# Kernel optimization log

Measured on AMD Instinct MI355X. Metric: run time of the kernel, lower is better.

The kernel has to match this reference:

```python
import jax, jax.numpy as jnp
import numpy as np

ROUTING_ITERS = 3
OUT_CAPS = 64
BETA_V = 1.0
BETA_A = 1.0
EPS = 1e-09


def l2_normalize(x, axis=-1, eps=1e-12):
    # matches tf.nn.l2_normalize: x / sqrt(max(sum(x^2), eps))
    sq = jnp.sum(jnp.square(x), axis=axis, keepdims=True)
    return x * jax.lax.rsqrt(jnp.maximum(sq, eps))


def setup_inputs() -> dict:
    key = jax.random.key(0)
    k1, k2 = jax.random.split(key)
    B, I, O, P = 32, 2048, OUT_CAPS, 16
    votes = jax.random.normal(k1, (B, I, O, P), dtype=jnp.float32)
    activations_in = jax.random.uniform(k2, (B, I), dtype=jnp.float32)
    return {"votes": votes, "activations_in": activations_in}


def reference(votes, activations_in):
    # votes: [B, I, O, P]; activations_in: [B, I]
    B, I, O, P = votes.shape
    A_h = jnp.full((B, O), 1.0 / O, dtype=votes.dtype)          # [B, O]
    Mu_h = l2_normalize(jnp.mean(votes, axis=1), axis=-1)        # [B, O, P]

    votes_norm = l2_normalize(votes, axis=-1)                    # [B, I, O, P]
    a_in = activations_in[:, :, None]                            # [B, I, 1]

    for _ in range(ROUTING_ITERS):
        # agreement cost
        dot = jnp.einsum('biop,bop->bio', votes_norm, Mu_h)      # [B, I, O]
        cost_v = (1.0 - jnp.square(dot)) * BETA_V
        cost_a = jnp.abs(a_in - A_h[:, None, :]) * BETA_A        # [B, I, O]
        log_posterior = -(cost_v + cost_a) + jnp.log(A_h + EPS)[:, None, :]
        R = jax.nn.softmax(log_posterior, axis=2)                # [B, I, O]

        # activation update
        R_sum = jnp.sum(R * a_in, axis=1)                        # [B, O]
        A_h = R_sum / (jnp.sum(R_sum, axis=1, keepdims=True) + EPS)
        A_h = jnp.clip(A_h, EPS, 1.0 - EPS)

        # pose update (weighted mean of votes)
        num = jnp.einsum('bio,biop->bop', R, votes)              # [B, O, P]
        den = jnp.sum(R, axis=1)[:, :, None] + EPS               # [B, O, 1]
        Mu_h = l2_normalize(num / den, axis=-1)

    return Mu_h, A_h
```

## Files before the change

kernel.cpp:

```cpp
#include <hip/hip_runtime.h>
#include <math.h>

#define NB 32
#define NI 2048
#define NO 64
#define NP 16
#define NBLK 32
#define EPSF 1e-9f

__device__ __forceinline__ float wave_sum64_shfl(float v) {
#pragma unroll
    for (int off = 32; off > 0; off >>= 1) v += __shfl_xor(v, off);
    return v;
}

__device__ __forceinline__ float wave_sum64_dpp(float v) {
    v += __int_as_float(__builtin_amdgcn_update_dpp(
        0, __float_as_int(v), 0x111, 0xf, 0xf, false));
    v += __int_as_float(__builtin_amdgcn_update_dpp(
        0, __float_as_int(v), 0x112, 0xf, 0xf, false));
    v += __int_as_float(__builtin_amdgcn_update_dpp(
        0, __float_as_int(v), 0x114, 0xf, 0xf, false));
    v += __int_as_float(__builtin_amdgcn_update_dpp(
        0, __float_as_int(v), 0x118, 0xf, 0xf, false));
    v += __int_as_float(__builtin_amdgcn_update_dpp(
        0, __float_as_int(v), 0x142, 0xa, 0xf, false));
    v += __int_as_float(__builtin_amdgcn_update_dpp(
        0, __float_as_int(v), 0x143, 0xc, 0xf, false));
    return __int_as_float(__builtin_amdgcn_readlane(__float_as_int(v), 63));
}

__global__ __launch_bounds__(256) void mean_accum_kernel(
        const float* __restrict__ votes, float* __restrict__ pm) {
    const int b    = blockIdx.y;
    const int bx   = blockIdx.x;
    const int wave = threadIdx.x >> 6;
    const int lane = threadIdx.x & 63;

    float s[NP];
#pragma unroll
    for (int p = 0; p < NP; ++p) s[p] = 0.f;

    const float* vbase =
        votes + (((size_t)b * NI + bx * 64 + wave) * NO + lane) * NP;
#pragma unroll 2
    for (int k = 0; k < 16; ++k) {
        const float4* vp =
            reinterpret_cast<const float4*>(vbase + (size_t)k * 4 * NO * NP);
        float4 v0 = vp[0], v1 = vp[1], v2 = vp[2], v3 = vp[3];
        s[0] += v0.x;  s[1] += v0.y;  s[2] += v0.z;  s[3] += v0.w;
        s[4] += v1.x;  s[5] += v1.y;  s[6] += v1.z;  s[7] += v1.w;
        s[8] += v2.x;  s[9] += v2.y;  s[10] += v2.z; s[11] += v2.w;
        s[12] += v3.x; s[13] += v3.y; s[14] += v3.z; s[15] += v3.w;
    }

    __shared__ float red[4][NO * NP];
#pragma unroll
    for (int p = 0; p < NP; ++p) red[wave][lane * NP + p] = s[p];
    __syncthreads();
    float* dst = pm + (size_t)(b * NBLK + bx) * (NO * NP);
    for (int e = threadIdx.x; e < NO * NP; e += 256)
        dst[e] = red[0][e] + red[1][e] + red[2][e] + red[3][e];
}

__global__ void mean_final_kernel(const float* __restrict__ pm,
                                  float* __restrict__ Mu, float* __restrict__ A) {
    const int b = blockIdx.x;
    const int o = threadIdx.x;
    float m[NP];
#pragma unroll
    for (int p = 0; p < NP; ++p) m[p] = 0.f;
    for (int bx = 0; bx < NBLK; ++bx) {
        const float4* q = reinterpret_cast<const float4*>(
            pm + (size_t)(b * NBLK + bx) * (NO * NP) + o * NP);
        float4 q0 = q[0], q1 = q[1], q2 = q[2], q3 = q[3];
        m[0] += q0.x;  m[1] += q0.y;  m[2] += q0.z;  m[3] += q0.w;
        m[4] += q1.x;  m[5] += q1.y;  m[6] += q1.z;  m[7] += q1.w;
        m[8] += q2.x;  m[9] += q2.y;  m[10] += q2.z; m[11] += q2.w;
        m[12] += q3.x; m[13] += q3.y; m[14] += q3.z; m[15] += q3.w;
    }
    float ssq = 0.f;
#pragma unroll
    for (int p = 0; p < NP; ++p) { m[p] *= (1.0f / NI); ssq += m[p] * m[p]; }
    float inv = rsqrtf(fmaxf(ssq, 1e-12f));
#pragma unroll
    for (int p = 0; p < NP; ++p)
        Mu[((size_t)b * NO + o) * NP + p] = m[p] * inv;
    A[b * NO + o] = 1.0f / (float)NO;
}

__global__ __launch_bounds__(256) void iter_accum_kernel(
        const float* __restrict__ votes, const float* __restrict__ act,
        const float* __restrict__ Mu, const float* __restrict__ A,
        float* __restrict__ ppn, float* __restrict__ ppd) {
    const int b    = blockIdx.y;
    const int bx   = blockIdx.x;
    const int wave = threadIdx.x >> 6;
    const int lane = threadIdx.x & 63;

    float mu[NP];
    {
        const float4* mp = reinterpret_cast<const float4*>(
            Mu + ((size_t)b * NO + lane) * NP);
        float4 m0 = mp[0], m1 = mp[1], m2 = mp[2], m3 = mp[3];
        mu[0] = m0.x;  mu[1] = m0.y;  mu[2] = m0.z;  mu[3] = m0.w;
        mu[4] = m1.x;  mu[5] = m1.y;  mu[6] = m1.z;  mu[7] = m1.w;
        mu[8] = m2.x;  mu[9] = m2.y;  mu[10] = m2.z; mu[11] = m2.w;
        mu[12] = m3.x; mu[13] = m3.y; mu[14] = m3.z; mu[15] = m3.w;
    }
    const float Ao   = A[b * NO + lane];
    const float logA = __logf(Ao + EPSF);

    float num[NP];
#pragma unroll
    for (int p = 0; p < NP; ++p) num[p] = 0.f;
    float den = 0.f, rs = 0.f;

    const float* vbase =
        votes + (((size_t)b * NI + bx * 64 + wave) * NO + lane) * NP;
    const float* abase = act + b * NI + bx * 64 + wave;

#pragma unroll 2
    for (int k = 0; k < 16; ++k) {
        const float4* vp =
            reinterpret_cast<const float4*>(vbase + (size_t)k * 4 * NO * NP);
        float4 v0 = vp[0], v1 = vp[1], v2 = vp[2], v3 = vp[3];

        float ssq = v0.x * v0.x + v0.y * v0.y + v0.z * v0.z + v0.w * v0.w
                  + v1.x * v1.x + v1.y * v1.y + v1.z * v1.z + v1.w * v1.w
                  + v2.x * v2.x + v2.y * v2.y + v2.z * v2.z + v2.w * v2.w
                  + v3.x * v3.x + v3.y * v3.y + v3.z * v3.z + v3.w * v3.w;
        float dt  = v0.x * mu[0]  + v0.y * mu[1]  + v0.z * mu[2]  + v0.w * mu[3]
                  + v1.x * mu[4]  + v1.y * mu[5]  + v1.z * mu[6]  + v1.w * mu[7]
                  + v2.x * mu[8]  + v2.y * mu[9]  + v2.z * mu[10] + v2.w * mu[11]
                  + v3.x * mu[12] + v3.y * mu[13] + v3.z * mu[14] + v3.w * mu[15];

        float dn = dt * __builtin_amdgcn_rsqf(fmaxf(ssq, 1e-12f));
        float a  = abase[4 * k];
        float lp = logA - (1.0f - dn * dn) - fabsf(a - Ao);
        float e  = __expf(lp);
        float R  = e * __builtin_amdgcn_rcpf(wave_sum64_dpp(e));

        rs  += R * a;
        den += R;
        num[0]  += R * v0.x; num[1]  += R * v0.y; num[2]  += R * v0.z; num[3]  += R * v0.w;
        num[4]  += R * v1.x; num[5]  += R * v1.y; num[6]  += R * v1.z; num[7]  += R * v1.w;
        num[8]  += R * v2.x; num[9]  += R * v2.y; num[10] += R * v2.z; num[11] += R * v2.w;
        num[12] += R * v3.x; num[13] += R * v3.y; num[14] += R * v3.z; num[15] += R * v3.w;
    }

    __shared__ float red[4][NO * 18];
    float* myred = &red[wave][lane * 18];
#pragma unroll
    for (int p = 0; p < NP; ++p) myred[p] = num[p];
    myred[16] = den;
    myred[17] = rs;
    __syncthreads();
    {
        float* dn_ = ppn + (size_t)(b * NBLK + bx) * (NO * NP);
        for (int e = threadIdx.x; e < NO * NP; e += 256) {
            int o = e >> 4, p = e & 15;
            dn_[e] = red[0][o * 18 + p] + red[1][o * 18 + p]
                   + red[2][o * 18 + p] + red[3][o * 18 + p];
        }
        float* dd_ = ppd + (size_t)(b * NBLK + bx) * (NO * 2);
        for (int e = threadIdx.x; e < NO * 2; e += 256) {
            int o = e >> 1, k = 16 + (e & 1);
            dd_[e] = red[0][o * 18 + k] + red[1][o * 18 + k]
                   + red[2][o * 18 + k] + red[3][o * 18 + k];
        }
    }
}

__global__ void finalize_kernel(const float* __restrict__ ppn,
                                const float* __restrict__ ppd,
                                float* __restrict__ Mu_out,
                                float* __restrict__ A_out) {
    const int b = blockIdx.x;
    const int o = threadIdx.x;
    float num[NP];
#pragma unroll
    for (int p = 0; p < NP; ++p) num[p] = 0.f;
    float den = 0.f, rs = 0.f;
    for (int bx = 0; bx < NBLK; ++bx) {
        const float4* q = reinterpret_cast<const float4*>(
            ppn + (size_t)(b * NBLK + bx) * (NO * NP) + o * NP);
        float4 q0 = q[0], q1 = q[1], q2 = q[2], q3 = q[3];
        num[0] += q0.x;  num[1] += q0.y;  num[2] += q0.z;  num[3] += q0.w;
        num[4] += q1.x;  num[5] += q1.y;  num[6] += q1.z;  num[7] += q1.w;
        num[8] += q2.x;  num[9] += q2.y;  num[10] += q2.z; num[11] += q2.w;
        num[12] += q3.x; num[13] += q3.y; num[14] += q3.z; num[15] += q3.w;
        const float2* d = reinterpret_cast<const float2*>(
            ppd + (size_t)(b * NBLK + bx) * (NO * 2) + o * 2);
        float2 dv = d[0];
        den += dv.x;
        rs  += dv.y;
    }
    float tot = wave_sum64_shfl(rs);
    float Anew = rs / (tot + EPSF);
    Anew = fminf(fmaxf(Anew, EPSF), 1.0f - EPSF);
    A_out[b * NO + o] = Anew;

    float inv_dn = 1.0f / (den + EPSF);
    float ssq = 0.f;
#pragma unroll
    for (int p = 0; p < NP; ++p) { num[p] *= inv_dn; ssq += num[p] * num[p]; }
    float inv = rsqrtf(fmaxf(ssq, 1e-12f));
#pragma unroll
    for (int p = 0; p < NP; ++p)
        Mu_out[((size_t)b * NO + o) * NP + p] = num[p] * inv;
}

extern "C" void kernel_launch(void* const* d_in, const int* in_sizes, int n_in,
                              void* d_out, int out_size, void* d_ws, size_t ws_size,
                              hipStream_t stream) {
    const float* votes = (const float*)d_in[0];
    const float* act   = (const float*)d_in[1];

    float* Mu_out = (float*)d_out;
    float* A_out  = (float*)d_out + NB * NO * NP;

    float* ws  = (float*)d_ws;
    float* ppn = ws;
    float* ppd = ws + NB * NBLK * 1024;
    float* Mu  = ppd + NB * NBLK * 128;
    float* A   = Mu + NB * NO * NP;

    dim3 grid(NBLK, NB);
    dim3 blk(256);

    mean_accum_kernel<<<grid, blk, 0, stream>>>(votes, ppn);
    mean_final_kernel<<<NB, NO, 0, stream>>>(ppn, Mu, A);

    for (int it = 0; it < 3; ++it) {
        iter_accum_kernel<<<grid, blk, 0, stream>>>(votes, act, Mu, A, ppn, ppd);
        float* mo = (it == 2) ? Mu_out : Mu;
        float* ao = (it == 2) ? A_out  : A;
        finalize_kernel<<<NB, NO, 0, stream>>>(ppn, ppd, mo, ao);
    }
}
```

Measured before the change: 512.8 us.

## Coalesce vote loads with quad-per-capsule mapping and finer I-blocking

Each lane now loads one float4 of a contiguous 1KB capsule row, so a wave's load is fully coalesced instead of each lane reading 64 strided bytes. Four lanes share one output capsule, and the dot products and squared norms are combined with DPP quad reductions. The I-block shrinks from 64 to 32, doubling the grid to 2048 blocks for more parallelism, and the finalize and mean kernels use 256 threads to reduce the partial sums. The trade-off is more partial-sum traffic and extra reduction instructions per vote.

```diff
diff --git a/kernel.cpp b/kernel.cpp
--- a/kernel.cpp
+++ b/kernel.cpp
@@ -5,7 +5,8 @@
 #define NI 2048
 #define NO 64
 #define NP 16
-#define NBLK 32
+#define IBLK 32
+#define NXB (NI / IBLK)
 #define EPSF 1e-9f
 
 __device__ __forceinline__ float wave_sum64_shfl(float v) {
@@ -14,201 +15,252 @@
     return v;
 }
 
+template <int CTRL, int RM, int BM>
+__device__ __forceinline__ float dppadd(float v) {
+    return v + __int_as_float(__builtin_amdgcn_update_dpp(
+        0, __float_as_int(v), CTRL, RM, BM, false));
+}
+
 __device__ __forceinline__ float wave_sum64_dpp(float v) {
-    v += __int_as_float(__builtin_amdgcn_update_dpp(
-        0, __float_as_int(v), 0x111, 0xf, 0xf, false));
-    v += __int_as_float(__builtin_amdgcn_update_dpp(
-        0, __float_as_int(v), 0x112, 0xf, 0xf, false));
-    v += __int_as_float(__builtin_amdgcn_update_dpp(
-        0, __float_as_int(v), 0x114, 0xf, 0xf, false));
-    v += __int_as_float(__builtin_amdgcn_update_dpp(
-        0, __float_as_int(v), 0x118, 0xf, 0xf, false));
-    v += __int_as_float(__builtin_amdgcn_update_dpp(
-        0, __float_as_int(v), 0x142, 0xa, 0xf, false));
-    v += __int_as_float(__builtin_amdgcn_update_dpp(
-        0, __float_as_int(v), 0x143, 0xc, 0xf, false));
+    v = dppadd<0x111, 0xf, 0xf>(v);
+    v = dppadd<0x112, 0xf, 0xf>(v);
+    v = dppadd<0x114, 0xf, 0xf>(v);
+    v = dppadd<0x118, 0xf, 0xf>(v);
+    v = dppadd<0x142, 0xa, 0xf>(v);
+    v = dppadd<0x143, 0xc, 0xf>(v);
     return __int_as_float(__builtin_amdgcn_readlane(__float_as_int(v), 63));
 }
 
+__device__ __forceinline__ float quad_sum4(float v) {
+    v = dppadd<0xB1, 0xf, 0xf>(v);
+    v = dppadd<0x4E, 0xf, 0xf>(v);
+    return v;
+}
+
 __global__ __launch_bounds__(256) void mean_accum_kernel(
-        const float* __restrict__ votes, float* __restrict__ pm) {
-    const int b    = blockIdx.y;
-    const int bx   = blockIdx.x;
-    const int wave = threadIdx.x >> 6;
-    const int lane = threadIdx.x & 63;
-
-    float s[NP];
-#pragma unroll
-    for (int p = 0; p < NP; ++p) s[p] = 0.f;
-
-    const float* vbase =
-        votes + (((size_t)b * NI + bx * 64 + wave) * NO + lane) * NP;
+        const float* __restrict__ votes, float* __restrict__ ppn) {
+    const int b  = blockIdx.y;
+    const int bx = blockIdx.x;
+    const int w  = threadIdx.x >> 6;
+    const int l  = threadIdx.x & 63;
+
+    const float4* vb = reinterpret_cast<const float4*>(votes)
+                     + (((size_t)b * NI + bx * IBLK + w * (IBLK / 4)) << 8) + l;
+
+    float s[16];
+#pragma unroll
+    for (int p = 0; p < 16; ++p) s[p] = 0.f;
+
 #pragma unroll 2
-    for (int k = 0; k < 16; ++k) {
-        const float4* vp =
-            reinterpret_cast<const float4*>(vbase + (size_t)k * 4 * NO * NP);
-        float4 v0 = vp[0], v1 = vp[1], v2 = vp[2], v3 = vp[3];
-        s[0] += v0.x;  s[1] += v0.y;  s[2] += v0.z;  s[3] += v0.w;
-        s[4] += v1.x;  s[5] += v1.y;  s[6] += v1.z;  s[7] += v1.w;
-        s[8] += v2.x;  s[9] += v2.y;  s[10] += v2.z; s[11] += v2.w;
+    for (int k = 0; k < IBLK / 4; ++k) {
+        const float4* pk = vb + ((size_t)k << 8);
+        float4 v0 = pk[0], v1 = pk[64], v2 = pk[128], v3 = pk[192];
+        s[0]  += v0.x; s[1]  += v0.y; s[2]  += v0.z; s[3]  += v0.w;
+        s[4]  += v1.x; s[5]  += v1.y; s[6]  += v1.z; s[7]  += v1.w;
+        s[8]  += v2.x; s[9]  += v2.y; s[10] += v2.z; s[11] += v2.w;
         s[12] += v3.x; s[13] += v3.y; s[14] += v3.z; s[15] += v3.w;
     }
 
     __shared__ float red[4][NO * NP];
-#pragma unroll
-    for (int p = 0; p < NP; ++p) red[wave][lane * NP + p] = s[p];
-    __syncthreads();
-    float* dst = pm + (size_t)(b * NBLK + bx) * (NO * NP);
+    float4* r4 = reinterpret_cast<float4*>(red[w]);
+    r4[0 * 64 + l] = make_float4(s[0], s[1], s[2], s[3]);
+    r4[1 * 64 + l] = make_float4(s[4], s[5], s[6], s[7]);
+    r4[2 * 64 + l] = make_float4(s[8], s[9], s[10], s[11]);
+    r4[3 * 64 + l] = make_float4(s[12], s[13], s[14], s[15]);
+    __syncthreads();
+    float* dst = ppn + (size_t)(b * NXB + bx) * (NO * NP);
     for (int e = threadIdx.x; e < NO * NP; e += 256)
         dst[e] = red[0][e] + red[1][e] + red[2][e] + red[3][e];
 }
 
-__global__ void mean_final_kernel(const float* __restrict__ pm,
-                                  float* __restrict__ Mu, float* __restrict__ A) {
+__global__ __launch_bounds__(256) void mean_final_kernel(
+        const float* __restrict__ ppn, float* __restrict__ Mu,
+        float* __restrict__ A) {
     const int b = blockIdx.x;
-    const int o = threadIdx.x;
-    float m[NP];
-#pragma unroll
-    for (int p = 0; p < NP; ++p) m[p] = 0.f;
-    for (int bx = 0; bx < NBLK; ++bx) {
+    const int w = threadIdx.x >> 6;
+    const int l = threadIdx.x & 63;
+
+    float m[16];
+#pragma unroll
+    for (int p = 0; p < 16; ++p) m[p] = 0.f;
+    for (int bx = w; bx < NXB; bx += 4) {
         const float4* q = reinterpret_cast<const float4*>(
-            pm + (size_t)(b * NBLK + bx) * (NO * NP) + o * NP);
+            ppn + (size_t)(b * NXB + bx) * (NO * NP) + l * NP);
         float4 q0 = q[0], q1 = q[1], q2 = q[2], q3 = q[3];
-        m[0] += q0.x;  m[1] += q0.y;  m[2] += q0.z;  m[3] += q0.w;
-        m[4] += q1.x;  m[5] += q1.y;  m[6] += q1.z;  m[7] += q1.w;
-        m[8] += q2.x;  m[9] += q2.y;  m[10] += q2.z; m[11] += q2.w;
+        m[0]  += q0.x; m[1]  += q0.y; m[2]  += q0.z; m[3]  += q0.w;
+        m[4]  += q1.x; m[5]  += q1.y; m[6]  += q1.z; m[7]  += q1.w;
+        m[8]  += q2.x; m[9]  += q2.y; m[10] += q2.z; m[11] += q2.w;
         m[12] += q3.x; m[13] += q3.y; m[14] += q3.z; m[15] += q3.w;
     }
-    float ssq = 0.f;
-#pragma unroll
-    for (int p = 0; p < NP; ++p) { m[p] *= (1.0f / NI); ssq += m[p] * m[p]; }
-    float inv = rsqrtf(fmaxf(ssq, 1e-12f));
-#pragma unroll
-    for (int p = 0; p < NP; ++p)
-        Mu[((size_t)b * NO + o) * NP + p] = m[p] * inv;
-    A[b * NO + o] = 1.0f / (float)NO;
+    __shared__ float red[4][NO * 17];
+#pragma unroll
+    for (int p = 0; p < 16; ++p) red[w][l * 17 + p] = m[p];
+    __syncthreads();
+    if (w == 0) {
+        float mm[16], ssq = 0.f;
+#pragma unroll
+        for (int p = 0; p < 16; ++p) {
+            mm[p] = (red[0][l * 17 + p] + red[1][l * 17 + p]
+                   + red[2][l * 17 + p] + red[3][l * 17 + p]) * (1.0f / NI);
+            ssq += mm[p] * mm[p];
+        }
+        float inv = rsqrtf(fmaxf(ssq, 1e-12f));
+        float4* mo = reinterpret_cast<float4*>(Mu + ((size_t)b * NO + l) * NP);
+        mo[0] = make_float4(mm[0] * inv, mm[1] * inv, mm[2] * inv, mm[3] * inv);
+        mo[1] = make_float4(mm[4] * inv, mm[5] * inv, mm[6] * inv, mm[7] * inv);
+        mo[2] = make_float4(mm[8] * inv, mm[9] * inv, mm[10] * inv, mm[11] * inv);
+        mo[3] = make_float4(mm[12] * inv, mm[13] * inv, mm[14] * inv, mm[15] * inv);
+        A[b * NO + l] = 1.0f / (float)NO;
+    }
 }
 
 __global__ __launch_bounds__(256) void iter_accum_kernel(
         const float* __restrict__ votes, const float* __restrict__ act,
         const float* __restrict__ Mu, const float* __restrict__ A,
         float* __restrict__ ppn, float* __restrict__ ppd) {
-    const int b    = blockIdx.y;
-    const int bx   = blockIdx.x;
-    const int wave = threadIdx.x >> 6;
-    const int lane = threadIdx.x & 63;
-
-    float mu[NP];
-    {
-        const float4* mp = reinterpret_cast<const float4*>(
-            Mu + ((size_t)b * NO + lane) * NP);
-        float4 m0 = mp[0], m1 = mp[1], m2 = mp[2], m3 = mp[3];
-        mu[0] = m0.x;  mu[1] = m0.y;  mu[2] = m0.z;  mu[3] = m0.w;
-        mu[4] = m1.x;  mu[5] = m1.y;  mu[6] = m1.z;  mu[7] = m1.w;
-        mu[8] = m2.x;  mu[9] = m2.y;  mu[10] = m2.z; mu[11] = m2.w;
-        mu[12] = m3.x; mu[13] = m3.y; mu[14] = m3.z; mu[15] = m3.w;
-    }
-    const float Ao   = A[b * NO + lane];
-    const float logA = __logf(Ao + EPSF);
-
-    float num[NP];
-#pragma unroll
-    for (int p = 0; p < NP; ++p) num[p] = 0.f;
-    float den = 0.f, rs = 0.f;
-
-    const float* vbase =
-        votes + (((size_t)b * NI + bx * 64 + wave) * NO + lane) * NP;
-    const float* abase = act + b * NI + bx * 64 + wave;
+    const int b  = blockIdx.y;
+    const int bx = blockIdx.x;
+    const int w  = threadIdx.x >> 6;
+    const int l  = threadIdx.x & 63;
+    const int qd = l >> 2;
+    const int pc = l & 3;
+
+    float mu[16], Ao[4], lA[4];
+#pragma unroll
+    for (int j = 0; j < 4; ++j) {
+        int o = 16 * j + qd;
+        float4 mv = reinterpret_cast<const float4*>(
+            Mu + ((size_t)b * NO + o) * NP)[pc];
+        mu[4 * j + 0] = mv.x; mu[4 * j + 1] = mv.y;
+        mu[4 * j + 2] = mv.z; mu[4 * j + 3] = mv.w;
+        Ao[j] = A[b * NO + o];
+        lA[j] = __logf(Ao[j] + EPSF);
+    }
+
+    float acc[16], den[4], rs[4];
+#pragma unroll
+    for (int p = 0; p < 16; ++p) acc[p] = 0.f;
+#pragma unroll
+    for (int j = 0; j < 4; ++j) { den[j] = 0.f; rs[j] = 0.f; }
+
+    const int i0 = bx * IBLK + w * (IBLK / 4);
+    const float4* vb = reinterpret_cast<const float4*>(votes)
+                     + (((size_t)b * NI + i0) << 8) + l;
+    const float* ab = act + b * NI + i0;
 
 #pragma unroll 2
-    for (int k = 0; k < 16; ++k) {
-        const float4* vp =
-            reinterpret_cast<const float4*>(vbase + (size_t)k * 4 * NO * NP);
-        float4 v0 = vp[0], v1 = vp[1], v2 = vp[2], v3 = vp[3];
-
-        float ssq = v0.x * v0.x + v0.y * v0.y + v0.z * v0.z + v0.w * v0.w
-                  + v1.x * v1.x + v1.y * v1.y + v1.z * v1.z + v1.w * v1.w
-                  + v2.x * v2.x + v2.y * v2.y + v2.z * v2.z + v2.w * v2.w
-                  + v3.x * v3.x + v3.y * v3.y + v3.z * v3.z + v3.w * v3.w;
-        float dt  = v0.x * mu[0]  + v0.y * mu[1]  + v0.z * mu[2]  + v0.w * mu[3]
-                  + v1.x * mu[4]  + v1.y * mu[5]  + v1.z * mu[6]  + v1.w * mu[7]
-                  + v2.x * mu[8]  + v2.y * mu[9]  + v2.z * mu[10] + v2.w * mu[11]
-                  + v3.x * mu[12] + v3.y * mu[13] + v3.z * mu[14] + v3.w * mu[15];
-
-        float dn = dt * __builtin_amdgcn_rsqf(fmaxf(ssq, 1e-12f));
-        float a  = abase[4 * k];
-        float lp = logA - (1.0f - dn * dn) - fabsf(a - Ao);
-        float e  = __expf(lp);
-        float R  = e * __builtin_amdgcn_rcpf(wave_sum64_dpp(e));
-
-        rs  += R * a;
-        den += R;
-        num[0]  += R * v0.x; num[1]  += R * v0.y; num[2]  += R * v0.z; num[3]  += R * v0.w;
-        num[4]  += R * v1.x; num[5]  += R * v1.y; num[6]  += R * v1.z; num[7]  += R * v1.w;
-        num[8]  += R * v2.x; num[9]  += R * v2.y; num[10] += R * v2.z; num[11] += R * v2.w;
-        num[12] += R * v3.x; num[13] += R * v3.y; num[14] += R * v3.z; num[15] += R * v3.w;
-    }
-
-    __shared__ float red[4][NO * 18];
-    float* myred = &red[wave][lane * 18];
-#pragma unroll
-    for (int p = 0; p < NP; ++p) myred[p] = num[p];
-    myred[16] = den;
-    myred[17] = rs;
-    __syncthreads();
-    {
-        float* dn_ = ppn + (size_t)(b * NBLK + bx) * (NO * NP);
-        for (int e = threadIdx.x; e < NO * NP; e += 256) {
-            int o = e >> 4, p = e & 15;
-            dn_[e] = red[0][o * 18 + p] + red[1][o * 18 + p]
-                   + red[2][o * 18 + p] + red[3][o * 18 + p];
+    for (int k = 0; k < IBLK / 4; ++k) {
+        const float4* pk = vb + ((size_t)k << 8);
+        float4 v0 = pk[0], v1 = pk[64], v2 = pk[128], v3 = pk[192];
+        float a = ab[k];
+
+        float dt0 = v0.x * mu[0]  + v0.y * mu[1]  + v0.z * mu[2]  + v0.w * mu[3];
+        float dt1 = v1.x * mu[4]  + v1.y * mu[5]  + v1.z * mu[6]  + v1.w * mu[7];
+        float dt2 = v2.x * mu[8]  + v2.y * mu[9]  + v2.z * mu[10] + v2.w * mu[11];
+        float dt3 = v3.x * mu[12] + v3.y * mu[13] + v3.z * mu[14] + v3.w * mu[15];
+        float sq0 = v0.x * v0.x + v0.y * v0.y + v0.z * v0.z + v0.w * v0.w;
+        float sq1 = v1.x * v1.x + v1.y * v1.y + v1.z * v1.z + v1.w * v1.w;
+        float sq2 = v2.x * v2.x + v2.y * v2.y + v2.z * v2.z + v2.w * v2.w;
+        float sq3 = v3.x * v3.x + v3.y * v3.y + v3.z * v3.z + v3.w * v3.w;
+
+        dt0 = quad_sum4(dt0); sq0 = quad_sum4(sq0);
+        dt1 = quad_sum4(dt1); sq1 = quad_sum4(sq1);
+        dt2 = quad_sum4(dt2); sq2 = quad_sum4(sq2);
+        dt3 = quad_sum4(dt3); sq3 = quad_sum4(sq3);
+
+        float e0 = __expf(lA[0] - (1.0f - dt0 * dt0 * __builtin_amdgcn_rcpf(fmaxf(sq0, 1e-12f))) - fabsf(a - Ao[0]));
+        float e1 = __expf(lA[1] - (1.0f - dt1 * dt1 * __builtin_amdgcn_rcpf(fmaxf(sq1, 1e-12f))) - fabsf(a - Ao[1]));
+        float e2 = __expf(lA[2] - (1.0f - dt2 * dt2 * __builtin_amdgcn_rcpf(fmaxf(sq2, 1e-12f))) - fabsf(a - Ao[2]));
+        float e3 = __expf(lA[3] - (1.0f - dt3 * dt3 * __builtin_amdgcn_rcpf(fmaxf(sq3, 1e-12f))) - fabsf(a - Ao[3]));
+
+        float S  = wave_sum64_dpp(e0 + e1 + e2 + e3) * 0.25f;
+        float ri = __builtin_amdgcn_rcpf(S);
+
+        float R0 = e0 * ri, R1 = e1 * ri, R2 = e2 * ri, R3 = e3 * ri;
+        den[0] += R0; den[1] += R1; den[2] += R2; den[3] += R3;
+        rs[0] += R0 * a; rs[1] += R1 * a; rs[2] += R2 * a; rs[3] += R3 * a;
+        acc[0]  += R0 * v0.x; acc[1]  += R0 * v0.y; acc[2]  += R0 * v0.z; acc[3]  += R0 * v0.w;
+        acc[4]  += R1 * v1.x; acc[5]  += R1 * v1.y; acc[6]  += R1 * v1.z; acc[7]  += R1 * v1.w;
+        acc[8]  += R2 * v2.x; acc[9]  += R2 * v2.y; acc[10] += R2 * v2.z; acc[11] += R2 * v2.w;
+        acc[12] += R3 * v3.x; acc[13] += R3 * v3.y; acc[14] += R3 * v3.z; acc[15] += R3 * v3.w;
+    }
+
+    __shared__ float redn[4][NO * NP];
+    __shared__ float redd[4][NO * 2];
+    float4* r4 = reinterpret_cast<float4*>(redn[w]);
+    r4[0 * 64 + l] = make_float4(acc[0], acc[1], acc[2], acc[3]);
+    r4[1 * 64 + l] = make_float4(acc[4], acc[5], acc[6], acc[7]);
+    r4[2 * 64 + l] = make_float4(acc[8], acc[9], acc[10], acc[11]);
+    r4[3 * 64 + l] = make_float4(acc[12], acc[13], acc[14], acc[15]);
+    if (pc == 0) {
+#pragma unroll
+        for (int j = 0; j < 4; ++j) {
+            int o = 16 * j + qd;
+            redd[w][o * 2 + 0] = den[j];
+            redd[w][o * 2 + 1] = rs[j];
         }
-        float* dd_ = ppd + (size_t)(b * NBLK + bx) * (NO * 2);
-        for (int e = threadIdx.x; e < NO * 2; e += 256) {
-            int o = e >> 1, k = 16 + (e & 1);
-            dd_[e] = red[0][o * 18 + k] + red[1][o * 18 + k]
-                   + red[2][o * 18 + k] + red[3][o * 18 + k];
+    }
+    __syncthreads();
+    float* dn_ = ppn + (size_t)(b * NXB + bx) * (NO * NP);
+    for (int e = threadIdx.x; e < NO * NP; e += 256)
+        dn_[e] = redn[0][e] + redn[1][e] + redn[2][e] + redn[3][e];
+    float* dd_ = ppd + (size_t)(b * NXB + bx) * (NO * 2);
+    for (int e = threadIdx.x; e < NO * 2; e += 256)
+        dd_[e] = redd[0][e] + redd[1][e] + redd[2][e] + redd[3][e];
+}
+
+__global__ __launch_bounds__(256) void finalize_kernel(
+        const float* __restrict__ ppn, const float* __restrict__ ppd,
+        float* __restrict__ Mu_out, float* __restrict__ A_out) {
+    const int b = blockIdx.x;
+    const int w = threadIdx.x >> 6;
+    const int l = threadIdx.x & 63;
+
+    float m[16], den = 0.f, rs = 0.f;
+#pragma unroll
+    for (int p = 0; p < 16; ++p) m[p] = 0.f;
+    for (int bx = w; bx < NXB; bx += 4) {
+        const float4* q = reinterpret_cast<const float4*>(
+            ppn + (size_t)(b * NXB + bx) * (NO * NP) + l * NP);
+        float4 q0 = q[0], q1 = q[1], q2 = q[2], q3 = q[3];
+        m[0]  += q0.x; m[1]  += q0.y; m[2]  += q0.z; m[3]  += q0.w;
+        m[4]  += q1.x; m[5]  += q1.y; m[6]  += q1.z; m[7]  += q1.w;
+        m[8]  += q2.x; m[9]  += q2.y; m[10] += q2.z; m[11] += q2.w;
+        m[12] += q3.x; m[13] += q3.y; m[14] += q3.z; m[15] += q3.w;
+        float2 d = reinterpret_cast<const float2*>(
+            ppd + (size_t)(b * NXB + bx) * (NO * 2))[l];
+        den += d.x; rs += d.y;
+    }
+    __shared__ float red[4][NO * 17];
+    __shared__ float redd2[4][NO * 2];
+#pragma unroll
+    for (int p = 0; p < 16; ++p) red[w][l * 17 + p] = m[p];
+    redd2[w][l * 2 + 0] = den;
+    redd2[w][l * 2 + 1] = rs;
+    __syncthreads();
+    if (w == 0) {
+        den = redd2[0][l * 2] + redd2[1][l * 2] + redd2[2][l * 2] + redd2[3][l * 2];
+        rs  = redd2[0][l * 2 + 1] + redd2[1][l * 2 + 1]
+            + redd2[2][l * 2 + 1] + redd2[3][l * 2 + 1];
+        float tot  = wave_sum64_shfl(rs);
+        float Anew = fminf(fmaxf(rs / (tot + EPSF), EPSF), 1.0f - EPSF);
+        A_out[b * NO + l] = Anew;
+
+        float invd = 1.0f / (den + EPSF);
+        float mm[16], ssq = 0.f;
+#pragma unroll
+        for (int p = 0; p < 16; ++p) {
+            mm[p] = (red[0][l * 17 + p] + red[1][l * 17 + p]
+                   + red[2][l * 17 + p] + red[3][l * 17 + p]) * invd;
+            ssq += mm[p] * mm[p];
         }
-    }
-}
-
-__global__ void finalize_kernel(const float* __restrict__ ppn,
-                                const float* __restrict__ ppd,
-                                float* __restrict__ Mu_out,
-                                float* __restrict__ A_out) {
-    const int b = blockIdx.x;
-    const int o = threadIdx.x;
-    float num[NP];
-#pragma unroll
-    for (int p = 0; p < NP; ++p) num[p] = 0.f;
-    float den = 0.f, rs = 0.f;
-    for (int bx = 0; bx < NBLK; ++bx) {
-        const float4* q = reinterpret_cast<const float4*>(
-            ppn + (size_t)(b * NBLK + bx) * (NO * NP) + o * NP);
-        float4 q0 = q[0], q1 = q[1], q2 = q[2], q3 = q[3];
-        num[0] += q0.x;  num[1] += q0.y;  num[2] += q0.z;  num[3] += q0.w;
-        num[4] += q1.x;  num[5] += q1.y;  num[6] += q1.z;  num[7] += q1.w;
-        num[8] += q2.x;  num[9] += q2.y;  num[10] += q2.z; num[11] += q2.w;
-        num[12] += q3.x; num[13] += q3.y; num[14] += q3.z; num[15] += q3.w;
-        const float2* d = reinterpret_cast<const float2*>(
-            ppd + (size_t)(b * NBLK + bx) * (NO * 2) + o * 2);
-        float2 dv = d[0];
-        den += dv.x;
-        rs  += dv.y;
-    }
-    float tot = wave_sum64_shfl(rs);
-    float Anew = rs / (tot + EPSF);
-    Anew = fminf(fmaxf(Anew, EPSF), 1.0f - EPSF);
-    A_out[b * NO + o] = Anew;
-
-    float inv_dn = 1.0f / (den + EPSF);
-    float ssq = 0.f;
-#pragma unroll
-    for (int p = 0; p < NP; ++p) { num[p] *= inv_dn; ssq += num[p] * num[p]; }
-    float inv = rsqrtf(fmaxf(ssq, 1e-12f));
-#pragma unroll
-    for (int p = 0; p < NP; ++p)
-        Mu_out[((size_t)b * NO + o) * NP + p] = num[p] * inv;
+        float inv = rsqrtf(fmaxf(ssq, 1e-12f));
+        float4* mo = reinterpret_cast<float4*>(Mu_out + ((size_t)b * NO + l) * NP);
+        mo[0] = make_float4(mm[0] * inv, mm[1] * inv, mm[2] * inv, mm[3] * inv);
+        mo[1] = make_float4(mm[4] * inv, mm[5] * inv, mm[6] * inv, mm[7] * inv);
+        mo[2] = make_float4(mm[8] * inv, mm[9] * inv, mm[10] * inv, mm[11] * inv);
+        mo[3] = make_float4(mm[12] * inv, mm[13] * inv, mm[14] * inv, mm[15] * inv);
+    }
 }
 
 extern "C" void kernel_launch(void* const* d_in, const int* in_sizes, int n_in,
@@ -222,20 +274,20 @@
 
     float* ws  = (float*)d_ws;
     float* ppn = ws;
-    float* ppd = ws + NB * NBLK * 1024;
-    float* Mu  = ppd + NB * NBLK * 128;
+    float* ppd = ws + (size_t)NB * NXB * (NO * NP);
+    float* Mu  = ppd + (size_t)NB * NXB * (NO * 2);
     float* A   = Mu + NB * NO * NP;
 
-    dim3 grid(NBLK, NB);
+    dim3 grid(NXB, NB);
     dim3 blk(256);
 
     mean_accum_kernel<<<grid, blk, 0, stream>>>(votes, ppn);
-    mean_final_kernel<<<NB, NO, 0, stream>>>(ppn, Mu, A);
+    mean_final_kernel<<<NB, blk, 0, stream>>>(ppn, Mu, A);
 
     for (int it = 0; it < 3; ++it) {
         iter_accum_kernel<<<grid, blk, 0, stream>>>(votes, act, Mu, A, ppn, ppd);
         float* mo = (it == 2) ? Mu_out : Mu;
         float* ao = (it == 2) ? A_out  : A;
-        finalize_kernel<<<NB, NO, 0, stream>>>(ppn, ppd, mo, ao);
-    }
-}
+        finalize_kernel<<<NB, blk, 0, stream>>>(ppn, ppd, mo, ao);
+    }
+}
```

Result: no change. 511.8 us (-0.2%).
